# Kernel tuning notes

Hardware: AMD Instinct MI355X
Metric: run time of the kernel (lower is better)

Reference implementation:

```python
import jax, jax.numpy as jnp
import numpy as np

B, T, C = 8, 2048, 1024
HEAD = 64

def setup_inputs() -> dict:
    key = jax.random.key(0)
    k1, k2, k3, k4 = jax.random.split(key, 4)
    x = jax.random.normal(k1, (B, T, C), dtype=jnp.float32)
    # nn.Linear(n_embed, head_size, bias=False): y = x @ W^T; store as [C, HEAD] for x @ W
    scale = 1.0 / np.sqrt(C)
    Wq = jax.random.normal(k2, (C, HEAD), dtype=jnp.float32) * scale
    Wk = jax.random.normal(k3, (C, HEAD), dtype=jnp.float32) * scale
    Wv = jax.random.normal(k4, (C, HEAD), dtype=jnp.float32) * scale
    return {"x": x, "Wq": Wq, "Wk": Wk, "Wv": Wv}

def reference(x, Wq, Wk, Wv):
    Bx, Tx, Cx = x.shape
    q = x @ Wq            # [B,T,H]
    k = x @ Wk            # [B,T,H]
    v = x @ Wv            # [B,T,H]
    # NOTE: original scales by C**-0.5 (embedding dim), not head_size**-0.5
    aff = jnp.einsum('bqh,bkh->bqk', q, k) * (Cx ** -0.5)  # [B,T,T]
    causal = jnp.tril(jnp.ones((Tx, Tx), dtype=bool))
    aff = jnp.where(causal, aff, -jnp.inf)
    probs = jax.nn.softmax(aff, axis=-1)
    # dropout p=0.0 (eval): identity
    return jnp.einsum('bqk,bkh->bqh', probs, v)
```

## Files before the change

kernel.cpp:

```cpp
#include <hip/hip_runtime.h>
#include <hip/hip_bf16.h>

typedef __attribute__((ext_vector_type(8))) short bf16x8;
typedef __attribute__((ext_vector_type(4))) float f32x4;
typedef __attribute__((ext_vector_type(4))) int i32x4;

#define LOG2E 1.4426950408889634f

static __device__ __forceinline__ unsigned int f2bfu(float f) {
    return (unsigned int)__builtin_bit_cast(unsigned short, __float2bfloat16(f));
}
static __device__ __forceinline__ unsigned int pack2(float lo, float hi) {
    return (f2bfu(hi) << 16) | f2bfu(lo);
}
static __device__ __forceinline__ unsigned short f2bf(float f) {
    return __builtin_bit_cast(unsigned short, __float2bfloat16(f));
}

__global__ __launch_bounds__(256) void wtrans_kernel(
    const float* __restrict__ Wq, const float* __restrict__ Wk,
    const float* __restrict__ Wv, unsigned short* __restrict__ Wts)
{
    const int part = blockIdx.x;
    const int t    = blockIdx.y;
    const int c    = part * 256 + threadIdx.x;
    const int n    = c >> 3;
    const int mat  = n >> 6;
    const int nl   = n & 63;
    const int k0   = t * 64 + (c & 7) * 8;
    const float* W = (mat == 0) ? Wq : ((mat == 1) ? Wk : Wv);
    const float scale = (mat == 0) ? 0.03125f : 1.0f;
    unsigned int s[8];
#pragma unroll
    for (int j = 0; j < 8; ++j)
        s[j] = (unsigned int)f2bf(W[(size_t)(k0 + j) * 64 + nl] * scale);
    i32x4 pk;
    pk[0] = (int)(s[0] | (s[1] << 16));
    pk[1] = (int)(s[2] | (s[3] << 16));
    pk[2] = (int)(s[4] | (s[5] << 16));
    pk[3] = (int)(s[6] | (s[7] << 16));
    *(i32x4*)(Wts + (size_t)t * 12288 + (size_t)c * 8) = pk;
}

__global__ __launch_bounds__(256, 2) void proj_kernel(
    const float* __restrict__ x, const unsigned short* __restrict__ Wts,
    unsigned short* __restrict__ Qb, unsigned short* __restrict__ Kp,
    unsigned short* __restrict__ Vp)
{
    __shared__ __align__(16) unsigned short sA[2][32][72];
    __shared__ __align__(16) unsigned short sB[2][192][72];
    __shared__ __align__(16) unsigned short sVT[64][48];
    __shared__ __align__(16) unsigned short sK[32][72];

    const int tid  = threadIdx.x;
    const int w    = tid >> 6;
    const int wm   = w >> 1;
    const int wn   = w & 1;
    const int lane = tid & 63;
    const int r    = lane & 15;
    const int g    = lane >> 4;
    const int mbase = blockIdx.x * 32;

    const int arow = tid >> 3;
    const int acb  = (tid & 7) * 8;
    const float* xptr = x + (size_t)(mbase + arow) * 1024 + acb;

    f32x4 acc[6];
#pragma unroll
    for (int i = 0; i < 6; ++i) acc[i] = (f32x4)0.0f;

    float4 XAa0, XAa1, XAb0, XAb1;
    i32x4 BB[6];

#define LOADX(S0, S1, t_) do { \
        const float* xp = xptr + (size_t)(t_) * 64; \
        S0 = *(const float4*)(xp);  S1 = *(const float4*)(xp + 4); \
    } while (0)

#define LOADB(t_) do { \
        const unsigned short* wp = Wts + (size_t)(t_) * 12288 + (size_t)tid * 8; \
        _Pragma("unroll") \
        for (int i = 0; i < 6; ++i) BB[i] = *(const i32x4*)(wp + i * 2048); \
    } while (0)

#define STORESTEP(buf, S0, S1) do { \
        i32x4 pa0 = {(int)pack2(S0.x, S0.y), (int)pack2(S0.z, S0.w), \
                     (int)pack2(S1.x, S1.y), (int)pack2(S1.z, S1.w)}; \
        *(i32x4*)&sA[buf][arow][acb] = pa0; \
        _Pragma("unroll") \
        for (int i = 0; i < 6; ++i) { \
            const int c = tid + 256 * i; \
            *(i32x4*)&sB[buf][c >> 3][(c & 7) * 8] = BB[i]; \
        } \
    } while (0)

#define COMPSTEP(buf) do { \
        _Pragma("unroll") \
        for (int h = 0; h < 2; ++h) { \
            bf16x8 af = *(const bf16x8*)&sA[buf][wm * 16 + r][h * 32 + g * 8]; \
            _Pragma("unroll") \
            for (int nt = 0; nt < 6; ++nt) { \
                bf16x8 bfr = *(const bf16x8*)&sB[buf][(nt * 2 + wn) * 16 + r][h * 32 + g * 8]; \
                acc[nt] = __builtin_amdgcn_mfma_f32_16x16x32_bf16(af, bfr, acc[nt], 0, 0, 0); \
            } \
        } \
    } while (0)

    LOADX(XAa0, XAa1, 0);
    LOADX(XAb0, XAb1, 1);
    LOADB(0);
#pragma unroll 1
    for (int t = 0; t < 16; t += 2) {
        STORESTEP(0, XAa0, XAa1);
        __syncthreads();
        if (t + 2 < 16) LOADX(XAa0, XAa1, t + 2);
        LOADB(t + 1);
        COMPSTEP(0);
        STORESTEP(1, XAb0, XAb1);
        __syncthreads();
        if (t + 3 < 16) LOADX(XAb0, XAb1, t + 3);
        if (t + 2 < 16) LOADB(t + 2);
        COMPSTEP(1);
    }

    const int row0  = mbase + wm * 16 + g * 4;
    const int lrow0 = wm * 16 + g * 4;
#pragma unroll
    for (int nt = 0; nt < 6; ++nt) {
        const int ti  = nt * 2 + wn;
        const int mat = ti >> 2;
        const int col = (ti & 3) * 16 + r;
#pragma unroll
        for (int j = 0; j < 4; ++j) {
            const float v = acc[nt][j];
            if (mat == 0) {
                Qb[(size_t)(row0 + j) * 64 + col] = f2bf(v);
            } else if (mat == 1) {
                sK[lrow0 + j][col] = f2bf(v);
            } else {
                sVT[col][lrow0 + j] = f2bf(v);
            }
        }
    }
    __syncthreads();
    {
        const int bb = mbase >> 11;
        const int t  = (mbase & 2047) >> 5;
        const int f  = tid >> 6;
        const int r2 = lane & 15, g2 = lane >> 4;
        const int krow = 8 * (r2 >> 2) + (r2 & 3) + (f >> 1) * 4;
        const int kcol = (f & 1) * 32 + g2 * 8;
        *(i32x4*)(Kp + ((size_t)(bb * 64 + t) * 4 + f) * 512 + lane * 8)
            = *(const i32x4*)&sK[krow][kcol];
        *(i32x4*)(Vp + ((size_t)(bb * 64 + t) * 4 + f) * 512 + lane * 8)
            = *(const i32x4*)&sVT[f * 16 + r2][g2 * 8];
    }
}

__global__ __launch_bounds__(512, 2) void attn_kernel(
    const unsigned short* __restrict__ Qb, const unsigned short* __restrict__ Kp,
    const unsigned short* __restrict__ Vp, float* __restrict__ out)
{
    __shared__ __align__(16) float sO[8][2][4][64][4];
    __shared__ float sM[8][2][16], sL[8][2][16];

    const int tid  = threadIdx.x;
    const int w    = tid >> 6;
    const int lane = tid & 63;
    const int r    = lane & 15;
    const int g    = lane >> 4;
    const int b    = blockIdx.x & 7;
    const int p    = blockIdx.x >> 3;
    const int qbL  = p * 32;
    const int qbH  = 2016 - p * 32;
    const int lastqL = qbL + 31;
    const int lastqH = qbH + 31;

    const unsigned short* Qbb = Qb + (size_t)b * 2048 * 64;
    const unsigned short* Kpb = Kp + (size_t)b * 64 * 2048;
    const unsigned short* Vpb = Vp + (size_t)b * 64 * 2048;

#define QBASE(qs) ((qs) < 2 ? (qbL + (qs) * 16) : (qbH + ((qs) - 2) * 16))

    bf16x8 qf[4][2];
#pragma unroll
    for (int qs = 0; qs < 4; ++qs)
#pragma unroll
        for (int h = 0; h < 2; ++h)
            qf[qs][h] = *(const bf16x8*)(Qbb + (size_t)(QBASE(qs) + r) * 64 + h * 32 + g * 8);

    f32x4 o[4][4];
#pragma unroll
    for (int qs = 0; qs < 4; ++qs)
#pragma unroll
        for (int i = 0; i < 4; ++i) o[qs][i] = (f32x4)0.0f;
    float m[4] = {-1e30f, -1e30f, -1e30f, -1e30f};
    float l[4] = {0.0f, 0.0f, 0.0f, 0.0f};

#define LOADK(K_, kvt) do { \
        const unsigned short* kp = Kpb + (size_t)(kvt) * 2048 + lane * 8; \
        K_[0] = *(const bf16x8*)(kp); \
        K_[1] = *(const bf16x8*)(kp + 512); \
        K_[2] = *(const bf16x8*)(kp + 1024); \
        K_[3] = *(const bf16x8*)(kp + 1536); \
    } while (0)
#define LOADV(V_, kvt) do { \
        const unsigned short* vp = Vpb + (size_t)(kvt) * 2048 + lane * 8; \
        _Pragma("unroll") \
        for (int i = 0; i < 4; ++i) V_[i] = *(const bf16x8*)(vp + i * 512); \
    } while (0)

    bf16x8 KA[4], VA[4];
#pragma unroll 1
    for (int kv0 = w * 32; kv0 <= lastqH; kv0 += 256) {
        const bool doLow = (kv0 <= lastqL);

        LOADK(KA, kv0 >> 5);
        LOADV(VA, kv0 >> 5);

        f32x4 s0[4], s1[4];
        __builtin_amdgcn_s_setprio(1);
#pragma unroll
        for (int qs = 0; qs < 4; ++qs) {
            s0[qs] = (f32x4)0.0f; s1[qs] = (f32x4)0.0f;
            if (qs < 2 && !doLow) continue;
            s0[qs] = __builtin_amdgcn_mfma_f32_16x16x32_bf16(KA[0], qf[qs][0], s0[qs], 0, 0, 0);
            s0[qs] = __builtin_amdgcn_mfma_f32_16x16x32_bf16(KA[1], qf[qs][1], s0[qs], 0, 0, 0);
            s1[qs] = __builtin_amdgcn_mfma_f32_16x16x32_bf16(KA[2], qf[qs][0], s1[qs], 0, 0, 0);
            s1[qs] = __builtin_amdgcn_mfma_f32_16x16x32_bf16(KA[3], qf[qs][1], s1[qs], 0, 0, 0);
        }
        __builtin_amdgcn_s_setprio(0);

        float lm[4] = {-1e30f, -1e30f, -1e30f, -1e30f};
#pragma unroll
        for (int qs = 0; qs < 4; ++qs) {
            if (qs < 2 && !doLow) continue;
            const int q = QBASE(qs) + r;
            if (kv0 + 31 > QBASE(qs)) {
#pragma unroll
                for (int j = 0; j < 4; ++j) {
                    if (kv0 + 8 * g + j > q)     s0[qs][j] = -1e30f;
                    if (kv0 + 8 * g + 4 + j > q) s1[qs][j] = -1e30f;
                }
            }
            lm[qs] = fmaxf(fmaxf(fmaxf(s0[qs][0], s0[qs][1]), fmaxf(s0[qs][2], s0[qs][3])),
                           fmaxf(fmaxf(s1[qs][0], s1[qs][1]), fmaxf(s1[qs][2], s1[qs][3])));
        }
        if (!__all(lm[0] <= m[0] + 8.0f && lm[1] <= m[1] + 8.0f &&
                   lm[2] <= m[2] + 8.0f && lm[3] <= m[3] + 8.0f)) {
#pragma unroll
            for (int qs = 0; qs < 4; ++qs) {
                float t2 = fmaxf(lm[qs], __shfl_xor(lm[qs], 16));
                t2 = fmaxf(t2, __shfl_xor(t2, 32));
                const float mn = fmaxf(m[qs], t2);
                const float alpha = __builtin_amdgcn_exp2f((m[qs] - mn) * LOG2E);
#pragma unroll
                for (int ht = 0; ht < 4; ++ht) o[qs][ht] *= alpha;
                l[qs] *= alpha;
                m[qs] = mn;
            }
        }

        __builtin_amdgcn_s_setprio(1);
#pragma unroll
        for (int qs = 0; qs < 4; ++qs) {
            if (qs < 2 && !doLow) continue;
            float p0[4], p1[4];
#pragma unroll
            for (int j = 0; j < 4; ++j) {
                p0[j] = __builtin_amdgcn_exp2f((s0[qs][j] - m[qs]) * LOG2E);
                p1[j] = __builtin_amdgcn_exp2f((s1[qs][j] - m[qs]) * LOG2E);
                l[qs] += p0[j] + p1[j];
            }
            i32x4 pw;
            pw[0] = (int)pack2(p0[0], p0[1]);
            pw[1] = (int)pack2(p0[2], p0[3]);
            pw[2] = (int)pack2(p1[0], p1[1]);
            pw[3] = (int)pack2(p1[2], p1[3]);
            bf16x8 pfrag = __builtin_bit_cast(bf16x8, pw);
            o[qs][0] = __builtin_amdgcn_mfma_f32_16x16x32_bf16(VA[0], pfrag, o[qs][0], 0, 0, 0);
            o[qs][1] = __builtin_amdgcn_mfma_f32_16x16x32_bf16(VA[1], pfrag, o[qs][1], 0, 0, 0);
            o[qs][2] = __builtin_amdgcn_mfma_f32_16x16x32_bf16(VA[2], pfrag, o[qs][2], 0, 0, 0);
            o[qs][3] = __builtin_amdgcn_mfma_f32_16x16x32_bf16(VA[3], pfrag, o[qs][3], 0, 0, 0);
        }
        __builtin_amdgcn_s_setprio(0);
    }

#define MERGE_STORE(QS, Q2) do { \
        float lr = l[QS]; \
        lr += __shfl_xor(lr, 16); \
        lr += __shfl_xor(lr, 32); \
        if (g == 0) { sM[w][Q2][r] = m[QS]; sL[w][Q2][r] = lr; } \
        _Pragma("unroll") \
        for (int ht = 0; ht < 4; ++ht) *(f32x4*)&sO[w][Q2][ht][lane][0] = o[QS][ht]; \
    } while (0)

#define MERGE_WRITE(QBASE0) do { \
        const int q2 = w >> 2, ht = w & 3; \
        float M = sM[0][q2][r]; \
        _Pragma("unroll") \
        for (int wp = 1; wp < 8; ++wp) M = fmaxf(M, sM[wp][q2][r]); \
        float L = 0.0f; \
        float beta[8]; \
        _Pragma("unroll") \
        for (int wp = 0; wp < 8; ++wp) { \
            beta[wp] = __builtin_amdgcn_exp2f((sM[wp][q2][r] - M) * LOG2E); \
            L += beta[wp] * sL[wp][q2][r]; \
        } \
        f32x4 av = (f32x4)0.0f; \
        _Pragma("unroll") \
        for (int wp = 0; wp < 8; ++wp) { \
            f32x4 t = *(const f32x4*)&sO[wp][q2][ht][lane][0]; \
            av += t * beta[wp]; \
        } \
        const float inv = 1.0f / L; \
        const int qrow = (QBASE0) + q2 * 16 + r; \
        *(f32x4*)(out + ((size_t)b * 2048 + qrow) * 64 + ht * 16 + g * 4) = av * inv; \
    } while (0)

    MERGE_STORE(0, 0);
    MERGE_STORE(1, 1);
    __syncthreads();
    MERGE_WRITE(qbL);
    __syncthreads();
    MERGE_STORE(2, 0);
    MERGE_STORE(3, 1);
    __syncthreads();
    MERGE_WRITE(qbH);
}

extern "C" void kernel_launch(void* const* d_in, const int* in_sizes, int n_in,
                              void* d_out, int out_size, void* d_ws, size_t ws_size,
                              hipStream_t stream) {
    const float* x  = (const float*)d_in[0];
    const float* Wq = (const float*)d_in[1];
    const float* Wk = (const float*)d_in[2];
    const float* Wv = (const float*)d_in[3];
    float* out = (float*)d_out;

    unsigned short* Qb  = (unsigned short*)d_ws;
    unsigned short* Kp  = Qb + (size_t)8 * 2048 * 64;
    unsigned short* Vp  = Kp + (size_t)8 * 64 * 2048;
    unsigned short* Wts = Vp + (size_t)8 * 64 * 2048;

    hipLaunchKernelGGL(wtrans_kernel, dim3(6, 16), dim3(256), 0, stream, Wq, Wk, Wv, Wts);
    hipLaunchKernelGGL(proj_kernel, dim3(512), dim3(256), 0, stream, x, Wts, Qb, Kp, Vp);
    hipLaunchKernelGGL(attn_kernel, dim3(256), dim3(512), 0, stream, Qb, Kp, Vp, out);
}
```

Before: 41.44 us.

## Read projection weights straight from global into MFMA operands, drop weight LDS staging

The projection kernel no longer stages the transposed weight tile in shared memory. Each of 8 waves (now 512 threads per block) loads its B fragments directly from global/L2 and owns one 16-column slice of Q, K and V, with 3 accumulators instead of 6. This cuts LDS footprint and store traffic so more blocks can be resident per CU. The cost is redundant global weight reads across the two row-waves, and weight-load latency now sits right before the MFMAs with no prefetch.

```diff
diff --git a/kernel.cpp b/kernel.cpp
--- a/kernel.cpp
+++ b/kernel.cpp
@@ -42,118 +42,99 @@
     *(i32x4*)(Wts + (size_t)t * 12288 + (size_t)c * 8) = pk;
 }
 
-__global__ __launch_bounds__(256, 2) void proj_kernel(
+__global__ __launch_bounds__(512, 4) void proj_kernel(
     const float* __restrict__ x, const unsigned short* __restrict__ Wts,
     unsigned short* __restrict__ Qb, unsigned short* __restrict__ Kp,
     unsigned short* __restrict__ Vp)
 {
     __shared__ __align__(16) unsigned short sA[2][32][72];
-    __shared__ __align__(16) unsigned short sB[2][192][72];
-    __shared__ __align__(16) unsigned short sVT[64][48];
+    __shared__ __align__(16) unsigned short sVT[64][40];
     __shared__ __align__(16) unsigned short sK[32][72];
 
     const int tid  = threadIdx.x;
     const int w    = tid >> 6;
-    const int wm   = w >> 1;
-    const int wn   = w & 1;
+    const int wm   = w >> 2;
+    const int wv   = w & 3;
     const int lane = tid & 63;
     const int r    = lane & 15;
     const int g    = lane >> 4;
     const int mbase = blockIdx.x * 32;
 
-    const int arow = tid >> 3;
-    const int acb  = (tid & 7) * 8;
+    const int arow = tid >> 4;
+    const int acb  = (tid & 15) * 4;
     const float* xptr = x + (size_t)(mbase + arow) * 1024 + acb;
 
-    f32x4 acc[6];
-#pragma unroll
-    for (int i = 0; i < 6; ++i) acc[i] = (f32x4)0.0f;
-
-    float4 XAa0, XAa1, XAb0, XAb1;
-    i32x4 BB[6];
-
-#define LOADX(S0, S1, t_) do { \
-        const float* xp = xptr + (size_t)(t_) * 64; \
-        S0 = *(const float4*)(xp);  S1 = *(const float4*)(xp + 4); \
-    } while (0)
-
-#define LOADB(t_) do { \
-        const unsigned short* wp = Wts + (size_t)(t_) * 12288 + (size_t)tid * 8; \
-        _Pragma("unroll") \
-        for (int i = 0; i < 6; ++i) BB[i] = *(const i32x4*)(wp + i * 2048); \
-    } while (0)
-
-#define STORESTEP(buf, S0, S1) do { \
-        i32x4 pa0 = {(int)pack2(S0.x, S0.y), (int)pack2(S0.z, S0.w), \
-                     (int)pack2(S1.x, S1.y), (int)pack2(S1.z, S1.w)}; \
-        *(i32x4*)&sA[buf][arow][acb] = pa0; \
-        _Pragma("unroll") \
-        for (int i = 0; i < 6; ++i) { \
-            const int c = tid + 256 * i; \
-            *(i32x4*)&sB[buf][c >> 3][(c & 7) * 8] = BB[i]; \
-        } \
-    } while (0)
-
-#define COMPSTEP(buf) do { \
-        _Pragma("unroll") \
-        for (int h = 0; h < 2; ++h) { \
-            bf16x8 af = *(const bf16x8*)&sA[buf][wm * 16 + r][h * 32 + g * 8]; \
-            _Pragma("unroll") \
-            for (int nt = 0; nt < 6; ++nt) { \
-                bf16x8 bfr = *(const bf16x8*)&sB[buf][(nt * 2 + wn) * 16 + r][h * 32 + g * 8]; \
-                acc[nt] = __builtin_amdgcn_mfma_f32_16x16x32_bf16(af, bfr, acc[nt], 0, 0, 0); \
-            } \
-        } \
-    } while (0)
-
-    LOADX(XAa0, XAa1, 0);
-    LOADX(XAb0, XAb1, 1);
-    LOADB(0);
+    f32x4 acc[3];
+#pragma unroll
+    for (int i = 0; i < 3; ++i) acc[i] = (f32x4)0.0f;
+
+    float4 Xa, Xb;
+
+#define PLOADX(S, t_) do { S = *(const float4*)(xptr + (size_t)(t_) * 64); } while (0)
+
+#define PSTORE(buf, S) do { \
+        unsigned long long pa = ((unsigned long long)pack2(S.z, S.w) << 32) \
+                              | (unsigned long long)pack2(S.x, S.y); \
+        *(unsigned long long*)&sA[buf][arow][acb] = pa; \
+    } while (0)
+
+#define PCOMP(buf, t_) do { \
+        const unsigned short* wp = Wts + (size_t)(t_) * 12288 + wv * 1024 + r * 64 + g * 8; \
+        bf16x8 b0 = *(const bf16x8*)(wp); \
+        bf16x8 b1 = *(const bf16x8*)(wp + 32); \
+        bf16x8 b2 = *(const bf16x8*)(wp + 4096); \
+        bf16x8 b3 = *(const bf16x8*)(wp + 4096 + 32); \
+        bf16x8 b4 = *(const bf16x8*)(wp + 8192); \
+        bf16x8 b5 = *(const bf16x8*)(wp + 8192 + 32); \
+        bf16x8 af0 = *(const bf16x8*)&sA[buf][wm * 16 + r][g * 8]; \
+        bf16x8 af1 = *(const bf16x8*)&sA[buf][wm * 16 + r][32 + g * 8]; \
+        acc[0] = __builtin_amdgcn_mfma_f32_16x16x32_bf16(af0, b0, acc[0], 0, 0, 0); \
+        acc[0] = __builtin_amdgcn_mfma_f32_16x16x32_bf16(af1, b1, acc[0], 0, 0, 0); \
+        acc[1] = __builtin_amdgcn_mfma_f32_16x16x32_bf16(af0, b2, acc[1], 0, 0, 0); \
+        acc[1] = __builtin_amdgcn_mfma_f32_16x16x32_bf16(af1, b3, acc[1], 0, 0, 0); \
+        acc[2] = __builtin_amdgcn_mfma_f32_16x16x32_bf16(af0, b4, acc[2], 0, 0, 0); \
+        acc[2] = __builtin_amdgcn_mfma_f32_16x16x32_bf16(af1, b5, acc[2], 0, 0, 0); \
+    } while (0)
+
+    PLOADX(Xa, 0);
+    PLOADX(Xb, 1);
 #pragma unroll 1
     for (int t = 0; t < 16; t += 2) {
-        STORESTEP(0, XAa0, XAa1);
+        PSTORE(0, Xa);
         __syncthreads();
-        if (t + 2 < 16) LOADX(XAa0, XAa1, t + 2);
-        LOADB(t + 1);
-        COMPSTEP(0);
-        STORESTEP(1, XAb0, XAb1);
+        if (t + 2 < 16) PLOADX(Xa, t + 2);
+        PCOMP(0, t);
+        PSTORE(1, Xb);
         __syncthreads();
-        if (t + 3 < 16) LOADX(XAb0, XAb1, t + 3);
-        if (t + 2 < 16) LOADB(t + 2);
-        COMPSTEP(1);
+        if (t + 3 < 16) PLOADX(Xb, t + 3);
+        PCOMP(1, t + 1);
     }
 
-    const int row0  = mbase + wm * 16 + g * 4;
-    const int lrow0 = wm * 16 + g * 4;
-#pragma unroll
-    for (int nt = 0; nt < 6; ++nt) {
-        const int ti  = nt * 2 + wn;
-        const int mat = ti >> 2;
-        const int col = (ti & 3) * 16 + r;
-#pragma unroll
-        for (int j = 0; j < 4; ++j) {
-            const float v = acc[nt][j];
-            if (mat == 0) {
-                Qb[(size_t)(row0 + j) * 64 + col] = f2bf(v);
-            } else if (mat == 1) {
-                sK[lrow0 + j][col] = f2bf(v);
-            } else {
-                sVT[col][lrow0 + j] = f2bf(v);
-            }
-        }
+    const int colw = wv * 16 + r;
+#pragma unroll
+    for (int j = 0; j < 4; ++j) {
+        const int lrow = wm * 16 + g * 4 + j;
+        Qb[(size_t)(mbase + lrow) * 64 + colw] = f2bf(acc[0][j]);
+        sK[lrow][colw]  = f2bf(acc[1][j]);
+        sVT[colw][lrow] = f2bf(acc[2][j]);
     }
     __syncthreads();
     {
         const int bb = mbase >> 11;
-        const int t  = (mbase & 2047) >> 5;
-        const int f  = tid >> 6;
-        const int r2 = lane & 15, g2 = lane >> 4;
-        const int krow = 8 * (r2 >> 2) + (r2 & 3) + (f >> 1) * 4;
-        const int kcol = (f & 1) * 32 + g2 * 8;
-        *(i32x4*)(Kp + ((size_t)(bb * 64 + t) * 4 + f) * 512 + lane * 8)
-            = *(const i32x4*)&sK[krow][kcol];
-        *(i32x4*)(Vp + ((size_t)(bb * 64 + t) * 4 + f) * 512 + lane * 8)
-            = *(const i32x4*)&sVT[f * 16 + r2][g2 * 8];
+        const int tt = (mbase & 2047) >> 5;
+        const int l2 = tid & 63;
+        const int r2 = l2 & 15, g2 = l2 >> 4;
+        if (tid < 256) {
+            const int f = tid >> 6;
+            const int krow = 8 * (r2 >> 2) + (r2 & 3) + (f >> 1) * 4;
+            const int kcol = (f & 1) * 32 + g2 * 8;
+            *(i32x4*)(Kp + ((size_t)(bb * 64 + tt) * 4 + f) * 512 + l2 * 8)
+                = *(const i32x4*)&sK[krow][kcol];
+        } else {
+            const int f = (tid - 256) >> 6;
+            *(i32x4*)(Vp + ((size_t)(bb * 64 + tt) * 4 + f) * 512 + l2 * 8)
+                = *(const i32x4*)&sVT[f * 16 + r2][g2 * 8];
+        }
     }
 }
 
@@ -344,6 +325,6 @@
     unsigned short* Wts = Vp + (size_t)8 * 64 * 2048;
 
     hipLaunchKernelGGL(wtrans_kernel, dim3(6, 16), dim3(256), 0, stream, Wq, Wk, Wv, Wts);
-    hipLaunchKernelGGL(proj_kernel, dim3(512), dim3(256), 0, stream, x, Wts, Qb, Kp, Vp);
+    hipLaunchKernelGGL(proj_kernel, dim3(512), dim3(512), 0, stream, x, Wts, Qb, Kp, Vp);
     hipLaunchKernelGGL(attn_kernel, dim3(256), dim3(512), 0, stream, Qb, Kp, Vp, out);
 }
```

Result: slower. 73.22 us (+76.7%).
